# Kernel optimization log

Measured on AMD Instinct MI355X. Metric: run time of the kernel, lower is better.

## Reference

```python
import jax, jax.numpy as jnp
import numpy as np

B, S, D = 2, 4096, 512
H, DQK, DV, W = 8, 64, 64, 32
ORDER = 6  # 2^(2*6)=4096 cells: 64x64 Hilbert grid covers max_seq_len=4096


def hilbert_d2xy(d, order):
    """Vectorized standard Hilbert curve d->(x,y) mapping on a 2^order grid."""
    x = jnp.zeros_like(d)
    y = jnp.zeros_like(d)
    t = d
    s = 1
    for _ in range(order):
        rx = (t // 2) & 1
        ry = (t ^ rx) & 1
        swap = ry == 0
        flip = swap & (rx == 1)
        xf = jnp.where(flip, s - 1 - x, x)
        yf = jnp.where(flip, s - 1 - y, y)
        x, y = jnp.where(swap, yf, xf), jnp.where(swap, xf, yf)
        x = x + s * rx
        y = y + s * ry
        t = t // 4
        s = s * 2
    return jnp.stack([x, y], axis=-1)


def neighbor_idx(seq_len, window):
    d = jnp.arange(seq_len, dtype=jnp.int32)
    coords = hilbert_d2xy(d, ORDER).astype(jnp.float32)  # (S, 2)
    diff = coords[:, None, :] - coords[None, :, :]
    dist = jnp.sqrt((diff ** 2).sum(-1))  # (S, S)
    _, idx = jax.lax.top_k(-dist, window)  # k smallest distances
    return idx.astype(jnp.int32)


def setup_inputs() -> dict:
    key = jax.random.key(0)
    k1, k2, k3, k4, k5 = jax.random.split(key, 5)
    sc = float(1.0 / np.sqrt(D))
    return {
        "x": jax.random.normal(k1, (B, S, D), jnp.float32),
        "W_q": jax.random.normal(k2, (H * DQK, D), jnp.float32) * sc,
        "W_k": jax.random.normal(k3, (H * DQK, D), jnp.float32) * sc,
        "W_v": jax.random.normal(k4, (H * DV, D), jnp.float32) * sc,
        "W_o": jax.random.normal(k5, (D, H * DV), jnp.float32) * sc,
        "neighbor_indices": neighbor_idx(S, W),
    }


def reference(x, W_q, W_k, W_v, W_o, neighbor_indices):
    b, s, _ = x.shape
    q = (x @ W_q.T).reshape(b, s, H, DQK).transpose(0, 2, 1, 3)  # (b,h,s,d)
    k = (x @ W_k.T).reshape(b, s, H, DQK).transpose(0, 2, 1, 3)
    v = (x @ W_v.T).reshape(b, s, H, DV).transpose(0, 2, 1, 3)
    kn = k[:, :, neighbor_indices, :]  # gather -> (b,h,s,w,d)
    vn = v[:, :, neighbor_indices, :]
    scale = float(1.0 / np.sqrt(DQK))
    scores = jnp.einsum('bhsd,bhswd->bhsw', q, kn) * scale
    attn = jax.nn.softmax(scores, axis=-1)
    out = jnp.einsum('bhsw,bhswd->bhsd', attn, vn)
    out = out.transpose(0, 2, 1, 3).reshape(b, s, H * DV)
    return out @ W_o.T
```

## Files before the change

### kernel.cpp

```cpp
#include <hip/hip_runtime.h>
#include <hip/hip_bf16.h>
#include <stdint.h>
#include <stddef.h>

constexpr int Bc = 2;
constexpr int Sc = 4096;
constexpr int Dc = 512;
constexpr int Hc = 8;
constexpr int Wc = 32;

using bf16_t = __bf16;
typedef __attribute__((ext_vector_type(8))) __bf16 bf16x8;
typedef __attribute__((ext_vector_type(4))) __bf16 bf16x4;
typedef __attribute__((ext_vector_type(4))) float f32x4;

__device__ __forceinline__ void async_copy16(const void* g, void* l) {
    __builtin_amdgcn_global_load_lds(
        (const __attribute__((address_space(1))) void*)g,
        (__attribute__((address_space(3))) void*)l,
        16, 0, 0);
}

__global__ void detect_dtype(const unsigned short* __restrict__ x16,
                             int* __restrict__ flag) {
    __shared__ int cnt;
    if (threadIdx.x == 0) cnt = 0;
    __syncthreads();
    int bad = 0;
    for (int i = threadIdx.x; i < 2048; i += 256) {
        unsigned e = (x16[i] >> 7) & 0xFFu;
        if (e == 0xFFu || e < 96u || e > 150u) bad++;
    }
    atomicAdd(&cnt, bad);
    __syncthreads();
    if (threadIdx.x == 0) *flag = (cnt > 100) ? 1 : 0;
}

__global__ void convert_x(const void* __restrict__ src, bf16_t* __restrict__ dst,
                          const int* __restrict__ flag) {
    const int i = (blockIdx.x * 256 + threadIdx.x) * 4;
    if (*flag) {
        const float4 v = *(const float4*)((const float*)src + i);
        bf16x4 o; o[0] = (bf16_t)v.x; o[1] = (bf16_t)v.y;
        o[2] = (bf16_t)v.z; o[3] = (bf16_t)v.w;
        *(bf16x4*)(dst + i) = o;
    } else {
        *(bf16x4*)(dst + i) = *(const bf16x4*)((const bf16_t*)src + i);
    }
}

__global__ void convert_w4(const void* __restrict__ s0, const void* __restrict__ s1,
                           const void* __restrict__ s2, const void* __restrict__ s3,
                           bf16_t* __restrict__ d0, bf16_t* __restrict__ d1,
                           bf16_t* __restrict__ d2, bf16_t* __restrict__ d3,
                           const int* __restrict__ flag) {
    const int which = blockIdx.x >> 8;
    const void* s = (which == 0) ? s0 : (which == 1) ? s1 : (which == 2) ? s2 : s3;
    bf16_t*    d  = (which == 0) ? d0 : (which == 1) ? d1 : (which == 2) ? d2 : d3;
    const int i = ((blockIdx.x & 255) * 256 + threadIdx.x) * 4;
    if (*flag) {
        const float4 v = *(const float4*)((const float*)s + i);
        bf16x4 o; o[0] = (bf16_t)v.x; o[1] = (bf16_t)v.y;
        o[2] = (bf16_t)v.z; o[3] = (bf16_t)v.w;
        *(bf16x4*)(d + i) = o;
    } else {
        *(bf16x4*)(d + i) = *(const bf16x4*)((const bf16_t*)s + i);
    }
}

template<int BM, int BN, int TM, int TN, bool F32OUT>
__global__ __launch_bounds__(256) void gemm_bt(
    const bf16_t* __restrict__ A, int lda,
    const bf16_t* __restrict__ B0, const bf16_t* __restrict__ B1,
    const bf16_t* __restrict__ B2, int ldb, int nPerB,
    void* __restrict__ C, int ldc, int K)
{
    constexpr int BK = 32;
    __shared__ __align__(1024) bf16_t Alds[BM * BK];
    __shared__ __align__(1024) bf16_t Blds[BN * BK];

    const int tid  = threadIdx.x;
    const int lane = tid & 63;
    const int wv   = tid >> 6;
    const int wm   = wv >> 1;
    const int wn   = wv & 1;
    const int r    = lane & 15;
    const int q4   = lane >> 4;

    const int blkM = blockIdx.x * BM;
    const int colC = blockIdx.y * BN;

    const bf16_t* Bp = B0;
    int nB = colC;
    if (nPerB > 0) {
        int wsel = colC / nPerB;
        nB = colC - wsel * nPerB;
        Bp = (wsel == 0) ? B0 : (wsel == 1) ? B1 : B2;
    }

    f32x4 acc[TM][TN];
    const f32x4 fzero = {0.f, 0.f, 0.f, 0.f};
    #pragma unroll
    for (int i = 0; i < TM; ++i)
        #pragma unroll
        for (int j = 0; j < TN; ++j) acc[i][j] = fzero;

    constexpr int A_LOADS = (BM * BK * 2) / (256 * 16);
    constexpr int B_LOADS = (BN * BK * 2) / (256 * 16);

    for (int kk = 0; kk < K; kk += BK) {
        __syncthreads();
        #pragma unroll
        for (int i = 0; i < A_LOADS; ++i) {
            int off  = i * 4096 + tid * 16;
            int row  = off >> 6;
            int colb = off & 63;
            const char* g = (const char*)A + ((size_t)(blkM + row) * lda + kk) * 2 + colb;
            async_copy16(g, (char*)Alds + off);
        }
        #pragma unroll
        for (int i = 0; i < B_LOADS; ++i) {
            int off  = i * 4096 + tid * 16;
            int row  = off >> 6;
            int colb = off & 63;
            const char* g = (const char*)Bp + ((size_t)(nB + row) * ldb + kk) * 2 + colb;
            async_copy16(g, (char*)Blds + off);
        }
        __syncthreads();

        bf16x8 af[TM], bfr[TN];
        #pragma unroll
        for (int mt = 0; mt < TM; ++mt)
            af[mt] = *(const bf16x8*)&Alds[(wm * TM * 16 + mt * 16 + r) * BK + q4 * 8];
        #pragma unroll
        for (int nt = 0; nt < TN; ++nt)
            bfr[nt] = *(const bf16x8*)&Blds[(wn * TN * 16 + nt * 16 + r) * BK + q4 * 8];

        #pragma unroll
        for (int mt = 0; mt < TM; ++mt)
            #pragma unroll
            for (int nt = 0; nt < TN; ++nt)
                acc[mt][nt] = __builtin_amdgcn_mfma_f32_16x16x32_bf16(
                    af[mt], bfr[nt], acc[mt][nt], 0, 0, 0);
    }

    #pragma unroll
    for (int mt = 0; mt < TM; ++mt) {
        #pragma unroll
        for (int nt = 0; nt < TN; ++nt) {
            int rr0 = blkM + wm * TM * 16 + mt * 16 + q4 * 4;
            int cc  = colC + wn * TN * 16 + nt * 16 + r;
            #pragma unroll
            for (int i = 0; i < 4; ++i) {
                size_t o = (size_t)(rr0 + i) * ldc + cc;
                if constexpr (F32OUT) ((float*)C)[o]  = acc[mt][nt][i];
                else                  ((bf16_t*)C)[o] = (bf16_t)acc[mt][nt][i];
            }
        }
    }
}

__global__ __launch_bounds__(256) void attn_fast(
    const bf16_t* __restrict__ QKV,
    const int*    __restrict__ nidx,
    bf16_t*       __restrict__ attn_out)
{
    __shared__ float wa_lds[4][64];
    const int lane = threadIdx.x & 63;
    const int wv   = threadIdx.x >> 6;

    const int bi  = blockIdx.x;
    const int blk = (bi & 7) * 2048 + (bi >> 3);
    const int wg  = blk * 4 + wv;
    const int s = wg & (Sc - 1);
    const int h = (wg >> 12) & (Hc - 1);
    const int b = wg >> 15;
    const size_t row = (size_t)b * Sc + s;

    const int w    = lane >> 1;
    const int half = lane & 1;
    const int t    = nidx[s * Wc + w];

    const char* qkvB  = (const char*)QKV;
    const char* Qptr  = qkvB + row * 3072 + h * 128 + half * 64;
    const char* Kptr  = qkvB + ((size_t)b * Sc + t) * 3072 + 1024 + h * 128 + half * 64;

    bf16x8 q8[4], k8[4];
    #pragma unroll
    for (int i = 0; i < 4; ++i) {
        q8[i] = *(const bf16x8*)(Qptr + 16 * i);
        k8[i] = *(const bf16x8*)(Kptr + 16 * i);
    }
    float p = 0.f;
    #pragma unroll
    for (int i = 0; i < 4; ++i)
        #pragma unroll
        for (int j = 0; j < 8; ++j)
            p += (float)q8[i][j] * (float)k8[i][j];
    p += __shfl_xor(p, 1);
    p *= 0.125f;

    float mx = p;
    #pragma unroll
    for (int m = 2; m <= 32; m <<= 1) mx = fmaxf(mx, __shfl_xor(mx, m));
    const float e = __expf(p - mx);
    float sum = e;
    #pragma unroll
    for (int m = 2; m <= 32; m <<= 1) sum += __shfl_xor(sum, m);
    const float a = e / sum;

    if (half == 0) {
        wa_lds[wv][2 * w]     = __int_as_float(t * 3072);
        wa_lds[wv][2 * w + 1] = a;
    }
    __syncthreads();

    const char* VbaseU = qkvB + (size_t)b * Sc * 3072 + 2048 + h * 128 + lane * 2;
    float acc = 0.f;
    #pragma unroll
    for (int w4 = 0; w4 < 8; ++w4) {
        const float4 c0 = *(const float4*)&wa_lds[wv][8 * w4];
        const float4 c1 = *(const float4*)&wa_lds[wv][8 * w4 + 4];
        acc = fmaf(c0.y, (float)*(const bf16_t*)(VbaseU + __float_as_int(c0.x)), acc);
        acc = fmaf(c0.w, (float)*(const bf16_t*)(VbaseU + __float_as_int(c0.z)), acc);
        acc = fmaf(c1.y, (float)*(const bf16_t*)(VbaseU + __float_as_int(c1.x)), acc);
        acc = fmaf(c1.w, (float)*(const bf16_t*)(VbaseU + __float_as_int(c1.z)), acc);
    }
    attn_out[row * 512 + h * 64 + lane] = (bf16_t)acc;
}

extern "C" void kernel_launch(void* const* d_in, const int* in_sizes, int n_in,
                              void* d_out, int out_size, void* d_ws, size_t ws_size,
                              hipStream_t stream) {
    (void)in_sizes; (void)n_in; (void)out_size; (void)ws_size;
    const int* nidx = (const int*)d_in[5];
    const int M = Bc * Sc;
    float* out = (float*)d_out;

    char* w = (char*)d_ws;
    int*    flag = (int*)w;
    bf16_t* xc   = (bf16_t*)(w + 256);
    bf16_t* Wqc  = xc  + 4194304;
    bf16_t* Wkc  = Wqc + 262144;
    bf16_t* Wvc  = Wkc + 262144;
    bf16_t* Woc  = Wvc + 262144;
    bf16_t* qkv  = Woc + 262144;
    bf16_t* attnS = xc;

    detect_dtype<<<1, 256, 0, stream>>>((const unsigned short*)d_in[0], flag);
    convert_x<<<4096, 256, 0, stream>>>(d_in[0], xc, flag);
    convert_w4<<<1024, 256, 0, stream>>>(d_in[1], d_in[2], d_in[3], d_in[4],
                                         Wqc, Wkc, Wvc, Woc, flag);

    gemm_bt<128, 128, 4, 4, false><<<dim3(M / 128, 1536 / 128), 256, 0, stream>>>(
        xc, Dc, Wqc, Wkc, Wvc, Dc, 512, qkv, 1536, Dc);

    attn_fast<<<(Bc * Hc * Sc) / 4, 256, 0, stream>>>(qkv, nidx, attnS);

    gemm_bt<64, 64, 2, 2, true><<<dim3(M / 64, 512 / 64), 256, 0, stream>>>(
        attnS, 512, Woc, Woc, Woc, 512, 0, out, Dc, Dc);
}
```

Measured before the change: 158.1 us.

## Merge conversion kernels, drop dtype detection, vectorize V gather, retile output GEMM

Removes the runtime dtype-detection kernel and folds the x and weight fp32-to-bf16 conversions into one launch, so inputs are now assumed to be fp32. The attention V accumulation now has each lane load two bf16 values as one 32-bit word over half the neighbours, then combines the two halves with a cross-lane shuffle. This halves the number of gather loads. The output projection GEMM switches to 128x64 tiles. Launch count and per-element load overhead drop, but the code loses the ability to handle bf16 inputs.

```diff
diff --git a/kernel.cpp b/kernel.cpp
--- a/kernel.cpp
+++ b/kernel.cpp
@@ -12,6 +12,7 @@
 using bf16_t = __bf16;
 typedef __attribute__((ext_vector_type(8))) __bf16 bf16x8;
 typedef __attribute__((ext_vector_type(4))) __bf16 bf16x4;
+typedef __attribute__((ext_vector_type(2))) __bf16 bf16x2;
 typedef __attribute__((ext_vector_type(4))) float f32x4;
 
 __device__ __forceinline__ void async_copy16(const void* g, void* l) {
@@ -21,51 +22,26 @@
         16, 0, 0);
 }
 
-__global__ void detect_dtype(const unsigned short* __restrict__ x16,
-                             int* __restrict__ flag) {
-    __shared__ int cnt;
-    if (threadIdx.x == 0) cnt = 0;
-    __syncthreads();
-    int bad = 0;
-    for (int i = threadIdx.x; i < 2048; i += 256) {
-        unsigned e = (x16[i] >> 7) & 0xFFu;
-        if (e == 0xFFu || e < 96u || e > 150u) bad++;
-    }
-    atomicAdd(&cnt, bad);
-    __syncthreads();
-    if (threadIdx.x == 0) *flag = (cnt > 100) ? 1 : 0;
-}
-
-__global__ void convert_x(const void* __restrict__ src, bf16_t* __restrict__ dst,
-                          const int* __restrict__ flag) {
-    const int i = (blockIdx.x * 256 + threadIdx.x) * 4;
-    if (*flag) {
-        const float4 v = *(const float4*)((const float*)src + i);
-        bf16x4 o; o[0] = (bf16_t)v.x; o[1] = (bf16_t)v.y;
-        o[2] = (bf16_t)v.z; o[3] = (bf16_t)v.w;
-        *(bf16x4*)(dst + i) = o;
-    } else {
-        *(bf16x4*)(dst + i) = *(const bf16x4*)((const bf16_t*)src + i);
-    }
-}
-
-__global__ void convert_w4(const void* __restrict__ s0, const void* __restrict__ s1,
-                           const void* __restrict__ s2, const void* __restrict__ s3,
-                           bf16_t* __restrict__ d0, bf16_t* __restrict__ d1,
-                           bf16_t* __restrict__ d2, bf16_t* __restrict__ d3,
-                           const int* __restrict__ flag) {
-    const int which = blockIdx.x >> 8;
-    const void* s = (which == 0) ? s0 : (which == 1) ? s1 : (which == 2) ? s2 : s3;
-    bf16_t*    d  = (which == 0) ? d0 : (which == 1) ? d1 : (which == 2) ? d2 : d3;
-    const int i = ((blockIdx.x & 255) * 256 + threadIdx.x) * 4;
-    if (*flag) {
-        const float4 v = *(const float4*)((const float*)s + i);
-        bf16x4 o; o[0] = (bf16_t)v.x; o[1] = (bf16_t)v.y;
-        o[2] = (bf16_t)v.z; o[3] = (bf16_t)v.w;
-        *(bf16x4*)(d + i) = o;
-    } else {
-        *(bf16x4*)(d + i) = *(const bf16x4*)((const bf16_t*)s + i);
-    }
+__global__ void convert_all(const float* __restrict__ x,
+                            const float* __restrict__ wq, const float* __restrict__ wk,
+                            const float* __restrict__ wv, const float* __restrict__ wo,
+                            bf16_t* __restrict__ xc, bf16_t* __restrict__ dq,
+                            bf16_t* __restrict__ dk, bf16_t* __restrict__ dv,
+                            bf16_t* __restrict__ dwo) {
+    const int blk = blockIdx.x;
+    const float* s; bf16_t* d; int base;
+    if (blk < 4096) { s = x; d = xc; base = blk * 1024; }
+    else {
+        const int r = blk - 4096, which = r >> 8;
+        s = (which == 0) ? wq : (which == 1) ? wk : (which == 2) ? wv : wo;
+        d = (which == 0) ? dq : (which == 1) ? dk : (which == 2) ? dv : dwo;
+        base = (r & 255) * 1024;
+    }
+    const int i = base + threadIdx.x * 4;
+    const float4 v = *(const float4*)(s + i);
+    bf16x4 o; o[0] = (bf16_t)v.x; o[1] = (bf16_t)v.y;
+    o[2] = (bf16_t)v.z; o[3] = (bf16_t)v.w;
+    *(bf16x4*)(d + i) = o;
 }
 
 template<int BM, int BN, int TM, int TN, bool F32OUT>
@@ -165,7 +141,7 @@
     const int*    __restrict__ nidx,
     bf16_t*       __restrict__ attn_out)
 {
-    __shared__ float wa_lds[4][64];
+    __shared__ __align__(16) float wa_lds[4][64];
     const int lane = threadIdx.x & 63;
     const int wv   = threadIdx.x >> 6;
 
@@ -181,9 +157,9 @@
     const int half = lane & 1;
     const int t    = nidx[s * Wc + w];
 
-    const char* qkvB  = (const char*)QKV;
-    const char* Qptr  = qkvB + row * 3072 + h * 128 + half * 64;
-    const char* Kptr  = qkvB + ((size_t)b * Sc + t) * 3072 + 1024 + h * 128 + half * 64;
+    const char* qkvB = (const char*)QKV;
+    const char* Qptr = qkvB + row * 3072 + h * 128 + half * 64;
+    const char* Kptr = qkvB + ((size_t)b * Sc + t) * 3072 + 1024 + h * 128 + half * 64;
 
     bf16x8 q8[4], k8[4];
     #pragma unroll
@@ -215,18 +191,33 @@
     }
     __syncthreads();
 
-    const char* VbaseU = qkvB + (size_t)b * Sc * 3072 + 2048 + h * 128 + lane * 2;
-    float acc = 0.f;
-    #pragma unroll
-    for (int w4 = 0; w4 < 8; ++w4) {
-        const float4 c0 = *(const float4*)&wa_lds[wv][8 * w4];
-        const float4 c1 = *(const float4*)&wa_lds[wv][8 * w4 + 4];
-        acc = fmaf(c0.y, (float)*(const bf16_t*)(VbaseU + __float_as_int(c0.x)), acc);
-        acc = fmaf(c0.w, (float)*(const bf16_t*)(VbaseU + __float_as_int(c0.z)), acc);
-        acc = fmaf(c1.y, (float)*(const bf16_t*)(VbaseU + __float_as_int(c1.x)), acc);
-        acc = fmaf(c1.w, (float)*(const bf16_t*)(VbaseU + __float_as_int(c1.z)), acc);
-    }
-    attn_out[row * 512 + h * 64 + lane] = (bf16_t)acc;
+    const int d2 = lane & 31;
+    const int nh = lane >> 5;
+    const float* chunkp = &wa_lds[wv][nh * 32];
+    const char* Vb = qkvB + (size_t)b * Sc * 3072 + 2048 + h * 128;
+    const int dk = d2 * 4;
+
+    float acc0 = 0.f, acc1 = 0.f;
+    #pragma unroll
+    for (int j = 0; j < 8; ++j) {
+        const float4 c = *(const float4*)(chunkp + 4 * j);
+        {
+            const unsigned v = *(const unsigned*)(Vb + __float_as_int(c.x) + dk);
+            acc0 = fmaf(c.y, __uint_as_float(v << 16), acc0);
+            acc1 = fmaf(c.y, __uint_as_float(v & 0xffff0000u), acc1);
+        }
+        {
+            const unsigned v = *(const unsigned*)(Vb + __float_as_int(c.z) + dk);
+            acc0 = fmaf(c.w, __uint_as_float(v << 16), acc0);
+            acc1 = fmaf(c.w, __uint_as_float(v & 0xffff0000u), acc1);
+        }
+    }
+    acc0 += __shfl_xor(acc0, 32);
+    acc1 += __shfl_xor(acc1, 32);
+    if (nh == 0) {
+        bf16x2 pr; pr[0] = (bf16_t)acc0; pr[1] = (bf16_t)acc1;
+        *(bf16x2*)((char*)attn_out + row * 1024 + h * 128 + dk) = pr;
+    }
 }
 
 extern "C" void kernel_launch(void* const* d_in, const int* in_sizes, int n_in,
@@ -238,7 +229,6 @@
     float* out = (float*)d_out;
 
     char* w = (char*)d_ws;
-    int*    flag = (int*)w;
     bf16_t* xc   = (bf16_t*)(w + 256);
     bf16_t* Wqc  = xc  + 4194304;
     bf16_t* Wkc  = Wqc + 262144;
@@ -247,16 +237,16 @@
     bf16_t* qkv  = Woc + 262144;
     bf16_t* attnS = xc;
 
-    detect_dtype<<<1, 256, 0, stream>>>((const unsigned short*)d_in[0], flag);
-    convert_x<<<4096, 256, 0, stream>>>(d_in[0], xc, flag);
-    convert_w4<<<1024, 256, 0, stream>>>(d_in[1], d_in[2], d_in[3], d_in[4],
-                                         Wqc, Wkc, Wvc, Woc, flag);
+    convert_all<<<5120, 256, 0, stream>>>(
+        (const float*)d_in[0], (const float*)d_in[1], (const float*)d_in[2],
+        (const float*)d_in[3], (const float*)d_in[4],
+        xc, Wqc, Wkc, Wvc, Woc);
 
     gemm_bt<128, 128, 4, 4, false><<<dim3(M / 128, 1536 / 128), 256, 0, stream>>>(
         xc, Dc, Wqc, Wkc, Wvc, Dc, 512, qkv, 1536, Dc);
 
     attn_fast<<<(Bc * Hc * Sc) / 4, 256, 0, stream>>>(qkv, nidx, attnS);
 
-    gemm_bt<64, 64, 2, 2, true><<<dim3(M / 64, 512 / 64), 256, 0, stream>>>(
+    gemm_bt<128, 64, 4, 2, true><<<dim3(M / 128, 512 / 64), 256, 0, stream>>>(
         attnS, 512, Woc, Woc, Woc, 512, 0, out, Dc, Dc);
 }
```

Measured after the change: 148.7 us. -5.9%, faster.
